# Kernel optimization log

Hardware: AMD Instinct MI355X
Metric: run time of the kernel (lower is better)

The kernel has to match this reference:

```python
import jax, jax.numpy as jnp
import numpy as np

N_BINS = 15
NUM_CLASSES = 16


def _risk_from_H2(u):
    # torch: 0.5*(1 - sqrt(clamp(2*2^-u - 1, min=0)))
    inner = 2.0 * jnp.exp2(-u) - 1.0
    pos = inner > 0.0
    s = jnp.sqrt(jnp.where(pos, inner, 1.0))  # safe sqrt (grad 0 where clamped)
    return 0.5 * (1.0 - jnp.where(pos, s, 0.0))


def setup_inputs() -> dict:
    key = jax.random.key(0)
    k1, k2 = jax.random.split(key)
    N = 4194304
    logits = jax.random.normal(k1, (N, NUM_CLASSES), dtype=jnp.float32)
    labels = jax.random.randint(k2, (N,), 0, NUM_CLASSES)
    return {"logits": logits, "labels": labels}


def reference(logits, labels):
    # logits: [N, C]; labels: [N]
    probs = jax.nn.softmax(logits, axis=-1)                     # [N, C]
    H2 = -jnp.log2((probs * probs).sum(-1) + 1e-12)             # [N]
    err_real = (jnp.argmax(probs, axis=-1) != labels).astype(H2.dtype)  # [N]

    # equal-frequency edges on detached H2 (linear-interp quantiles, as torch.quantile)
    q = jnp.linspace(0.0, 1.0, N_BINS + 1)
    edges = jnp.quantile(jax.lax.stop_gradient(H2), q)
    edges = edges.at[-1].add(1e-6)
    lo, hi = edges[:-1], edges[1:]                              # [n_bins]

    # vectorized replacement of the per-bin Python loop: [n_bins, N] mask
    mask = (H2[None, :] > lo[:, None]) & (H2[None, :] <= hi[:, None])
    maskf = mask.astype(H2.dtype)
    cnt = maskf.sum(-1)                                         # [n_bins]
    safe = jnp.maximum(cnt, 1.0)
    u_bar = (maskf @ H2) / safe                                 # masked means
    err_bar = (maskf @ err_real) / safe
    gaps = jnp.where(cnt > 0.0, jnp.abs(err_bar - _risk_from_H2(u_bar)), 0.0)
    return gaps.mean()
```

## Files before the change

kernel.cpp:

```cpp
#include <hip/hip_runtime.h>

#define L1_BINS 8192
#define L2_BINS 512
#define KEY_MAX 4194303u
#define NH2_BLOCKS 1280
#define NREF_BLOCKS 512
#define NBIN_BLOCKS 256

struct Ranks { unsigned int r[32]; };
struct Fracs { float f[16]; };

__global__ __launch_bounds__(256) void k_zero(uint4* __restrict__ p, int n4) {
  int i = blockIdx.x * blockDim.x + threadIdx.x;
  if (i < n4) p[i] = make_uint4(0u, 0u, 0u, 0u);
}

__global__ __launch_bounds__(256) void k_h2(const float* __restrict__ logits,
                                            const int* __restrict__ labels,
                                            unsigned int* __restrict__ keys,
                                            unsigned int* __restrict__ histg,
                                            int n) {
  __shared__ unsigned int lh[L1_BINS];
  for (int i = threadIdx.x; i < L1_BINS; i += blockDim.x) lh[i] = 0u;
  __syncthreads();
  int tid = blockIdx.x * blockDim.x + threadIdx.x;
  int sub = tid & 3;
  int group = tid >> 2;
  int ngroups = (gridDim.x * blockDim.x) >> 2;
  for (int row = group; row < n; row += ngroups) {
    float4 v = reinterpret_cast<const float4*>(logits)[(size_t)row * 4 + sub];
    float m = v.x; int a = 0;
    if (v.y > m) { m = v.y; a = 1; }
    if (v.z > m) { m = v.z; a = 2; }
    if (v.w > m) { m = v.w; a = 3; }
    int gidx = sub * 4 + a;
#pragma unroll
    for (int mask = 1; mask <= 2; mask <<= 1) {
      float om = __shfl_xor(m, mask);
      int oi = __shfl_xor(gidx, mask);
      if (om > m || (om == m && oi < gidx)) { m = om; gidx = oi; }
    }
    float e0 = __expf(v.x - m), e1 = __expf(v.y - m);
    float e2 = __expf(v.z - m), e3 = __expf(v.w - m);
    float Z = e0 + e1 + e2 + e3;
    float S2 = e0 * e0 + e1 * e1 + e2 * e2 + e3 * e3;
#pragma unroll
    for (int mask = 1; mask <= 2; mask <<= 1) {
      Z += __shfl_xor(Z, mask);
      S2 += __shfl_xor(S2, mask);
    }
    if (sub == 0) {
      float r = S2 / (Z * Z) + 1e-12f;
      float h2 = -__log2f(r);
      int ki = (int)(h2 * 1048576.0f);
      unsigned int key = (unsigned int)min(max(ki, 0), (int)KEY_MAX);
      unsigned int err = (gidx != labels[row]) ? 0x80000000u : 0u;
      keys[row] = key | err;
      atomicAdd(&lh[key >> 9], 1u);
    }
  }
  __syncthreads();
  unsigned int* dst = histg + (size_t)blockIdx.x * (L1_BINS / 2);
  for (int i = threadIdx.x; i < L1_BINS / 2; i += blockDim.x)
    dst[i] = (lh[2 * i] & 0xFFFFu) | (lh[2 * i + 1] << 16);
}

__global__ __launch_bounds__(256) void k_merge(const unsigned int* __restrict__ histg,
                                               unsigned int* __restrict__ merged,
                                               int nrows) {
  __shared__ unsigned int slo[16][17], shi[16][17];
  int col0 = blockIdx.x * 16;
  int c = threadIdx.x & 15;
  int rg = threadIdx.x >> 4;
  unsigned int alo = 0, ahi = 0;
  for (int r = rg; r < nrows; r += 16) {
    unsigned int v = histg[(size_t)r * (L1_BINS / 2) + col0 + c];
    alo += v & 0xFFFFu;
    ahi += v >> 16;
  }
  slo[rg][c] = alo;
  shi[rg][c] = ahi;
  __syncthreads();
  if (threadIdx.x < 16) {
    unsigned int lo = 0, hi = 0;
#pragma unroll
    for (int g = 0; g < 16; ++g) { lo += slo[g][threadIdx.x]; hi += shi[g][threadIdx.x]; }
    int pc = col0 + threadIdx.x;
    merged[2 * pc] = lo;
    merged[2 * pc + 1] = hi;
  }
}

__global__ void k_select(const unsigned int* __restrict__ hist,
                         unsigned int* __restrict__ selpfx,
                         unsigned int* __restrict__ selrank,
                         float* __restrict__ vout,
                         int nb, int perq, int shift, int last, int first,
                         Ranks rk) {
  int j = blockIdx.x;
  int lane = threadIdx.x;
  const unsigned int* h = hist + (perq ? (size_t)j * (size_t)nb : (size_t)0);
  unsigned int rem = first ? rk.r[j] : selrank[j];
  int base = 0, len = nb;
  while (len > 64) {
    int chunk = (len + 63) >> 6;
    int start = base + lane * chunk;
    int end = base + len;
    unsigned int s = 0;
    for (int t = 0; t < chunk; ++t) {
      int idx = start + t;
      if (idx < end) s += h[idx];
    }
    unsigned int inc = s;
#pragma unroll
    for (int d = 1; d < 64; d <<= 1) {
      unsigned int u = __shfl_up(inc, d);
      if (lane >= d) inc += u;
    }
    unsigned int ex = inc - s;
    bool own = (rem >= ex) && (rem < ex + s);
    unsigned long long bal = __ballot(own);
    int src = __ffsll((long long)bal) - 1;
    unsigned int exs = __shfl(ex, src);
    int nbase = base + src * chunk;
    len = min(chunk, end - nbase);
    base = nbase;
    rem -= exs;
  }
  unsigned int s = (lane < len) ? h[base + lane] : 0u;
  unsigned int inc = s;
#pragma unroll
  for (int d = 1; d < 64; d <<= 1) {
    unsigned int u = __shfl_up(inc, d);
    if (lane >= d) inc += u;
  }
  unsigned int ex = inc - s;
  bool own = (rem >= ex) && (rem < ex + s);
  unsigned long long bal = __ballot(own);
  int src = __ffsll((long long)bal) - 1;
  unsigned int exs = __shfl(ex, src);
  if (lane == 0) {
    unsigned int idx = (unsigned int)(base + src);
    unsigned int pfx = first ? idx : ((selpfx[j] << shift) | idx);
    selpfx[j] = pfx;
    selrank[j] = rem - exs;
    if (last) vout[j] = __uint_as_float(pfx);
  }
}

__global__ __launch_bounds__(256) void k_refine(const unsigned int* __restrict__ keys,
                                                const unsigned int* __restrict__ selpfx,
                                                unsigned int* __restrict__ hist2,
                                                int n) {
  __shared__ unsigned int sp[32];
  if (threadIdx.x < 32) sp[threadIdx.x] = selpfx[threadIdx.x];
  __syncthreads();
  int stride = gridDim.x * blockDim.x;
  for (int i = blockIdx.x * blockDim.x + threadIdx.x; i < n; i += stride) {
    unsigned int key = keys[i] & KEY_MAX;
    unsigned int hi = key >> 9;
    unsigned int sub = key & (L2_BINS - 1);
#pragma unroll
    for (int jj = 0; jj < 32; ++jj) {
      if (hi == sp[jj]) atomicAdd(&hist2[jj * L2_BINS + (int)sub], 1u);
    }
  }
}

__global__ __launch_bounds__(256) void k_bin(const unsigned int* __restrict__ keys,
                                             const float* __restrict__ vp,
                                             float* __restrict__ partials,
                                             unsigned int* __restrict__ done,
                                             float* __restrict__ out, int n,
                                             Fracs fr) {
  __shared__ float sedge[16];
  __shared__ float swacc[4][48];
  __shared__ unsigned int is_last;
  if (threadIdx.x < 16) {
    int i = threadIdx.x;
    unsigned int klo = __float_as_uint(vp[2 * i]);
    unsigned int khi = __float_as_uint(vp[2 * i + 1]);
    float lo = (float)(klo + 1u) * 0x1p-20f;
    float hi = (float)(khi + 1u) * 0x1p-20f;
    float f = fr.f[i];
    float e = lo * (1.0f - f) + hi * f;
    if (i == 15) e += 1e-6f;
    sedge[i] = e;
  }
  __syncthreads();
  float e[16];
#pragma unroll
  for (int j = 0; j < 16; ++j) e[j] = sedge[j];
  float cnt[15], sH[15], sE[15];
#pragma unroll
  for (int b = 0; b < 15; ++b) { cnt[b] = 0.f; sH[b] = 0.f; sE[b] = 0.f; }
  int stride = gridDim.x * blockDim.x;
  for (int i = blockIdx.x * blockDim.x + threadIdx.x; i < n; i += stride) {
    unsigned int kp = keys[i];
    float h = ((float)(kp & KEY_MAX) + 0.5f) * 0x1p-20f;
    float er = (kp & 0x80000000u) ? 1.0f : 0.0f;
    int less = 0;
#pragma unroll
    for (int j = 0; j < 16; ++j) less += (h > e[j]) ? 1 : 0;
    int bin = less - 1;
#pragma unroll
    for (int b = 0; b < 15; ++b) {
      bool m = (bin == b);
      cnt[b] += m ? 1.f : 0.f;
      sH[b] += m ? h : 0.f;
      sE[b] += m ? er : 0.f;
    }
  }
  int wid = threadIdx.x >> 6;
  int lane = threadIdx.x & 63;
#pragma unroll
  for (int b = 0; b < 15; ++b) {
    float c = cnt[b], a = sH[b], s = sE[b];
    for (int off = 32; off > 0; off >>= 1) {
      c += __shfl_xor(c, off);
      a += __shfl_xor(a, off);
      s += __shfl_xor(s, off);
    }
    if (lane == 0) {
      swacc[wid][b] = c;
      swacc[wid][15 + b] = a;
      swacc[wid][30 + b] = s;
    }
  }
  __syncthreads();
  if (threadIdx.x < 45) {
    int v = threadIdx.x;
    float s = swacc[0][v] + swacc[1][v] + swacc[2][v] + swacc[3][v];
    partials[v * NBIN_BLOCKS + blockIdx.x] = s;
  }
  __threadfence();
  if (threadIdx.x == 0)
    is_last = (atomicAdd(done, 1u) == (unsigned int)gridDim.x - 1u) ? 1u : 0u;
  __syncthreads();
  if (is_last && threadIdx.x < 64) {
    __shared__ float sacc[45];
    int l = threadIdx.x;
    for (int v = 0; v < 45; ++v) {
      float s = 0.f;
      for (int b = l; b < NBIN_BLOCKS; b += 64) s += partials[v * NBIN_BLOCKS + b];
      for (int off = 32; off > 0; off >>= 1) s += __shfl_xor(s, off);
      if (l == 0) sacc[v] = s;
    }
    __builtin_amdgcn_s_barrier();
    float g = 0.f;
    if (l < 15) {
      float c = sacc[l], sh = sacc[15 + l], se = sacc[30 + l];
      float safe = fmaxf(c, 1.f);
      float u = sh / safe, eb = se / safe;
      float inner = 2.0f * exp2f(-u) - 1.0f;
      float s = (inner > 0.f) ? sqrtf(inner) : 0.f;
      float risk = 0.5f * (1.0f - s);
      g = (c > 0.f) ? fabsf(eb - risk) : 0.f;
    }
    for (int off = 32; off > 0; off >>= 1) g += __shfl_xor(g, off);
    if (l == 0) out[0] = g * (1.0f / 15.0f);
  }
}

extern "C" void kernel_launch(void* const* d_in, const int* in_sizes, int n_in,
                              void* d_out, int out_size, void* d_ws, size_t ws_size,
                              hipStream_t stream) {
  const float* logits = (const float*)d_in[0];
  const int* labels = (const int*)d_in[1];
  float* out = (float*)d_out;
  int n = in_sizes[1];

  char* ws = (char*)d_ws;
  size_t offKeys = 0;
  size_t offHg = (size_t)n * 4;
  size_t offMerged = offHg + (size_t)NH2_BLOCKS * (L1_BINS / 2) * 4;
  size_t offH2b = offMerged + (size_t)L1_BINS * 4;
  size_t offDone = offH2b + 32 * L2_BINS * 4;
  size_t zeroEnd = offDone + 16;
  size_t offSelP = zeroEnd;
  size_t offSelR = offSelP + 128;
  size_t offV = offSelR + 128;
  size_t offPart = (offV + 128 + 255) & ~(size_t)255;

  unsigned int* keys = (unsigned int*)(ws + offKeys);
  unsigned int* histg = (unsigned int*)(ws + offHg);
  unsigned int* merged = (unsigned int*)(ws + offMerged);
  unsigned int* hist2 = (unsigned int*)(ws + offH2b);
  unsigned int* done = (unsigned int*)(ws + offDone);
  unsigned int* selp = (unsigned int*)(ws + offSelP);
  unsigned int* selr = (unsigned int*)(ws + offSelR);
  float* vp = (float*)(ws + offV);
  float* part = (float*)(ws + offPart);

  Ranks rk;
  Fracs fr;
  float nm1 = (float)(n - 1);
  for (int i = 0; i < 16; ++i) {
    float q = (i == 15) ? 1.0f : (float)i * (1.0f / 15.0f);
    float idxf = q * nm1;
    float flo = floorf(idxf);
    unsigned int klo = (unsigned int)flo;
    unsigned int khi = (unsigned int)ceilf(idxf);
    unsigned int maxi = (unsigned int)(n - 1);
    if (klo > maxi) klo = maxi;
    if (khi > maxi) khi = maxi;
    rk.r[2 * i] = klo;
    rk.r[2 * i + 1] = khi;
    fr.f[i] = idxf - flo;
  }

  int zero4 = (int)((zeroEnd - offH2b) >> 4);
  k_zero<<<(zero4 + 255) / 256, 256, 0, stream>>>((uint4*)(ws + offH2b), zero4);
  k_h2<<<NH2_BLOCKS, 256, 0, stream>>>(logits, labels, keys, histg, n);
  k_merge<<<L1_BINS / 2 / 16, 256, 0, stream>>>(histg, merged, NH2_BLOCKS);
  k_select<<<32, 64, 0, stream>>>(merged, selp, selr, vp, L1_BINS, 0, 0, 0, 1, rk);
  k_refine<<<NREF_BLOCKS, 256, 0, stream>>>(keys, selp, hist2, n);
  k_select<<<32, 64, 0, stream>>>(hist2, selp, selr, vp, L2_BINS, 1, 9, 1, 0, rk);
  k_bin<<<NBIN_BLOCKS, 256, 0, stream>>>(keys, vp, part, done, out, n, fr);

  (void)n_in; (void)out_size; (void)ws_size;
}
```

Baseline: 317.1 us.

## Fuse select passes into merge/refine via last-block pattern, rebalance histogram bins

Removes the zero kernel and both standalone select kernels. Zeroing of counters and the level-2 histogram moves into k_h2 and k_merge, and each radix-select step runs in the last-arriving block of k_merge or k_refine, detected with an atomic counter. The L1 histogram shrinks to 4096 bins packed two per uint, written with one atomic per row, and L2 grows to 1024 bins. Grid sizes for the h2, refine and bin kernels go up. This cuts launch count and serialization, at the cost of more per-block histogram partials to merge and tail work done by a single block.

```diff
diff --git a/kernel.cpp b/kernel.cpp
--- a/kernel.cpp
+++ b/kernel.cpp
@@ -1,32 +1,41 @@
 #include <hip/hip_runtime.h>
 
-#define L1_BINS 8192
-#define L2_BINS 512
+#define L1_BINS 4096
+#define L1_UINTS 2048
+#define L2_BINS 1024
 #define KEY_MAX 4194303u
-#define NH2_BLOCKS 1280
-#define NREF_BLOCKS 512
-#define NBIN_BLOCKS 256
+#define NH2_BLOCKS 2048
+#define NMG_BLOCKS 256
+#define NREF_BLOCKS 2048
+#define NBIN_BLOCKS 1024
 
 struct Ranks { unsigned int r[32]; };
 struct Fracs { float f[16]; };
 
-__global__ __launch_bounds__(256) void k_zero(uint4* __restrict__ p, int n4) {
-  int i = blockIdx.x * blockDim.x + threadIdx.x;
-  if (i < n4) p[i] = make_uint4(0u, 0u, 0u, 0u);
+__device__ __forceinline__ unsigned int wave_iscan(unsigned int s, int lane) {
+  unsigned int inc = s;
+#pragma unroll
+  for (int d = 1; d < 64; d <<= 1) {
+    unsigned int u = __shfl_up(inc, d);
+    if (lane >= d) inc += u;
+  }
+  return inc;
 }
 
 __global__ __launch_bounds__(256) void k_h2(const float* __restrict__ logits,
                                             const int* __restrict__ labels,
                                             unsigned int* __restrict__ keys,
                                             unsigned int* __restrict__ histg,
+                                            unsigned int* __restrict__ dones,
                                             int n) {
-  __shared__ unsigned int lh[L1_BINS];
-  for (int i = threadIdx.x; i < L1_BINS; i += blockDim.x) lh[i] = 0u;
-  __syncthreads();
-  int tid = blockIdx.x * blockDim.x + threadIdx.x;
+  __shared__ unsigned int lh[L1_UINTS];
+  for (int i = threadIdx.x; i < L1_UINTS; i += 256) lh[i] = 0u;
+  if (blockIdx.x == 0 && threadIdx.x < 3) dones[threadIdx.x] = 0u;
+  __syncthreads();
+  int tid = blockIdx.x * 256 + threadIdx.x;
   int sub = tid & 3;
   int group = tid >> 2;
-  int ngroups = (gridDim.x * blockDim.x) >> 2;
+  int ngroups = (gridDim.x * 256) >> 2;
   for (int row = group; row < n; row += ngroups) {
     float4 v = reinterpret_cast<const float4*>(logits)[(size_t)row * 4 + sub];
     float m = v.x; int a = 0;
@@ -54,123 +63,132 @@
       float h2 = -__log2f(r);
       int ki = (int)(h2 * 1048576.0f);
       unsigned int key = (unsigned int)min(max(ki, 0), (int)KEY_MAX);
-      unsigned int err = (gidx != labels[row]) ? 0x80000000u : 0u;
-      keys[row] = key | err;
-      atomicAdd(&lh[key >> 9], 1u);
-    }
-  }
-  __syncthreads();
-  unsigned int* dst = histg + (size_t)blockIdx.x * (L1_BINS / 2);
-  for (int i = threadIdx.x; i < L1_BINS / 2; i += blockDim.x)
-    dst[i] = (lh[2 * i] & 0xFFFFu) | (lh[2 * i + 1] << 16);
+      keys[row] = key | ((gidx != labels[row]) ? 0x80000000u : 0u);
+      atomicAdd(&lh[key >> 11], ((key >> 10) & 1u) ? 65536u : 1u);
+    }
+  }
+  __syncthreads();
+  unsigned int* dst = histg + (size_t)blockIdx.x * L1_UINTS;
+  for (int i = threadIdx.x; i < L1_UINTS; i += 256) dst[i] = lh[i];
 }
 
 __global__ __launch_bounds__(256) void k_merge(const unsigned int* __restrict__ histg,
                                                unsigned int* __restrict__ merged,
-                                               int nrows) {
-  __shared__ unsigned int slo[16][17], shi[16][17];
-  int col0 = blockIdx.x * 16;
-  int c = threadIdx.x & 15;
-  int rg = threadIdx.x >> 4;
+                                               unsigned int* __restrict__ hist2,
+                                               unsigned int* __restrict__ dones,
+                                               unsigned int* __restrict__ selpfx,
+                                               unsigned int* __restrict__ selrank,
+                                               Ranks rk) {
+  __shared__ unsigned int slo[32][9], shi[32][9];
+  __shared__ unsigned int is_last;
+  for (int i = threadIdx.x; i < 128; i += 256)
+    hist2[blockIdx.x * 128 + i] = 0u;
+  int col0 = blockIdx.x * 8;
+  int c = threadIdx.x & 7;
+  int rg = threadIdx.x >> 3;
   unsigned int alo = 0, ahi = 0;
-  for (int r = rg; r < nrows; r += 16) {
-    unsigned int v = histg[(size_t)r * (L1_BINS / 2) + col0 + c];
+  for (int r = rg; r < NH2_BLOCKS; r += 32) {
+    unsigned int v = histg[(size_t)r * L1_UINTS + col0 + c];
     alo += v & 0xFFFFu;
     ahi += v >> 16;
   }
   slo[rg][c] = alo;
   shi[rg][c] = ahi;
   __syncthreads();
-  if (threadIdx.x < 16) {
+  if (threadIdx.x < 8) {
     unsigned int lo = 0, hi = 0;
 #pragma unroll
-    for (int g = 0; g < 16; ++g) { lo += slo[g][threadIdx.x]; hi += shi[g][threadIdx.x]; }
+    for (int g = 0; g < 32; ++g) { lo += slo[g][threadIdx.x]; hi += shi[g][threadIdx.x]; }
     int pc = col0 + threadIdx.x;
     merged[2 * pc] = lo;
     merged[2 * pc + 1] = hi;
   }
-}
-
-__global__ void k_select(const unsigned int* __restrict__ hist,
-                         unsigned int* __restrict__ selpfx,
-                         unsigned int* __restrict__ selrank,
-                         float* __restrict__ vout,
-                         int nb, int perq, int shift, int last, int first,
-                         Ranks rk) {
-  int j = blockIdx.x;
-  int lane = threadIdx.x;
-  const unsigned int* h = hist + (perq ? (size_t)j * (size_t)nb : (size_t)0);
-  unsigned int rem = first ? rk.r[j] : selrank[j];
-  int base = 0, len = nb;
-  while (len > 64) {
-    int chunk = (len + 63) >> 6;
-    int start = base + lane * chunk;
-    int end = base + len;
+  __threadfence();
+  __syncthreads();
+  if (threadIdx.x == 0)
+    is_last = (atomicAdd(&dones[0], 1u) == (unsigned int)gridDim.x - 1u) ? 1u : 0u;
+  __syncthreads();
+  if (!is_last) return;
+  __threadfence();
+  int wid = threadIdx.x >> 6, lane = threadIdx.x & 63;
+  for (int j = wid; j < 32; j += 4) {
+    unsigned int rem = rk.r[j];
+    const unsigned int* mp = merged + lane * 64;
     unsigned int s = 0;
-    for (int t = 0; t < chunk; ++t) {
-      int idx = start + t;
-      if (idx < end) s += h[idx];
-    }
-    unsigned int inc = s;
-#pragma unroll
-    for (int d = 1; d < 64; d <<= 1) {
-      unsigned int u = __shfl_up(inc, d);
-      if (lane >= d) inc += u;
-    }
+#pragma unroll 8
+    for (int t = 0; t < 64; ++t) s += mp[t];
+    unsigned int inc = wave_iscan(s, lane);
     unsigned int ex = inc - s;
     bool own = (rem >= ex) && (rem < ex + s);
-    unsigned long long bal = __ballot(own);
-    int src = __ffsll((long long)bal) - 1;
-    unsigned int exs = __shfl(ex, src);
-    int nbase = base + src * chunk;
-    len = min(chunk, end - nbase);
-    base = nbase;
-    rem -= exs;
-  }
-  unsigned int s = (lane < len) ? h[base + lane] : 0u;
-  unsigned int inc = s;
-#pragma unroll
-  for (int d = 1; d < 64; d <<= 1) {
-    unsigned int u = __shfl_up(inc, d);
-    if (lane >= d) inc += u;
-  }
-  unsigned int ex = inc - s;
-  bool own = (rem >= ex) && (rem < ex + s);
-  unsigned long long bal = __ballot(own);
-  int src = __ffsll((long long)bal) - 1;
-  unsigned int exs = __shfl(ex, src);
-  if (lane == 0) {
-    unsigned int idx = (unsigned int)(base + src);
-    unsigned int pfx = first ? idx : ((selpfx[j] << shift) | idx);
-    selpfx[j] = pfx;
-    selrank[j] = rem - exs;
-    if (last) vout[j] = __uint_as_float(pfx);
+    int src = __ffsll((long long)__ballot(own)) - 1;
+    rem -= __shfl(ex, src);
+    int base = src * 64;
+    unsigned int v2 = merged[base + lane];
+    unsigned int inc2 = wave_iscan(v2, lane);
+    unsigned int ex2 = inc2 - v2;
+    bool own2 = (rem >= ex2) && (rem < ex2 + v2);
+    int s2 = __ffsll((long long)__ballot(own2)) - 1;
+    unsigned int ex2s = __shfl(ex2, s2);
+    if (lane == 0) {
+      selpfx[j] = (unsigned int)(base + s2);
+      selrank[j] = rem - ex2s;
+    }
   }
 }
 
 __global__ __launch_bounds__(256) void k_refine(const unsigned int* __restrict__ keys,
                                                 const unsigned int* __restrict__ selpfx,
                                                 unsigned int* __restrict__ hist2,
+                                                unsigned int* __restrict__ dones,
+                                                unsigned int* __restrict__ selrank,
+                                                unsigned int* __restrict__ vout,
                                                 int n) {
   __shared__ unsigned int sp[32];
+  __shared__ unsigned int is_last;
   if (threadIdx.x < 32) sp[threadIdx.x] = selpfx[threadIdx.x];
   __syncthreads();
   int stride = gridDim.x * blockDim.x;
   for (int i = blockIdx.x * blockDim.x + threadIdx.x; i < n; i += stride) {
     unsigned int key = keys[i] & KEY_MAX;
-    unsigned int hi = key >> 9;
-    unsigned int sub = key & (L2_BINS - 1);
-#pragma unroll
-    for (int jj = 0; jj < 32; ++jj) {
-      if (hi == sp[jj]) atomicAdd(&hist2[jj * L2_BINS + (int)sub], 1u);
-    }
+    unsigned int hi = key >> 10;
+    unsigned int sb = key & (L2_BINS - 1);
+#pragma unroll
+    for (int jj = 0; jj < 32; ++jj)
+      if (hi == sp[jj]) atomicAdd(&hist2[jj * L2_BINS + (int)sb], 1u);
+  }
+  __threadfence();
+  __syncthreads();
+  if (threadIdx.x == 0)
+    is_last = (atomicAdd(&dones[1], 1u) == (unsigned int)gridDim.x - 1u) ? 1u : 0u;
+  __syncthreads();
+  if (!is_last) return;
+  __threadfence();
+  int wid = threadIdx.x >> 6, lane = threadIdx.x & 63;
+  for (int j = wid; j < 32; j += 4) {
+    unsigned int rem = selrank[j];
+    const unsigned int* h = hist2 + j * L2_BINS;
+    unsigned int s = 0;
+#pragma unroll
+    for (int t = 0; t < 16; ++t) s += h[lane * 16 + t];
+    unsigned int inc = wave_iscan(s, lane);
+    unsigned int ex = inc - s;
+    bool own = (rem >= ex) && (rem < ex + s);
+    int src = __ffsll((long long)__ballot(own)) - 1;
+    rem -= __shfl(ex, src);
+    unsigned int v2 = (lane < 16) ? h[src * 16 + lane] : 0u;
+    unsigned int inc2 = wave_iscan(v2, lane);
+    unsigned int ex2 = inc2 - v2;
+    bool own2 = (lane < 16) && (rem >= ex2) && (rem < ex2 + v2);
+    int s2 = __ffsll((long long)__ballot(own2)) - 1;
+    if (lane == 0)
+      vout[j] = (sp[j] << 10) | (unsigned int)(src * 16 + s2);
   }
 }
 
 __global__ __launch_bounds__(256) void k_bin(const unsigned int* __restrict__ keys,
-                                             const float* __restrict__ vp,
+                                             const unsigned int* __restrict__ vp,
                                              float* __restrict__ partials,
-                                             unsigned int* __restrict__ done,
+                                             unsigned int* __restrict__ dones,
                                              float* __restrict__ out, int n,
                                              Fracs fr) {
   __shared__ float sedge[16];
@@ -178,8 +196,8 @@
   __shared__ unsigned int is_last;
   if (threadIdx.x < 16) {
     int i = threadIdx.x;
-    unsigned int klo = __float_as_uint(vp[2 * i]);
-    unsigned int khi = __float_as_uint(vp[2 * i + 1]);
+    unsigned int klo = vp[2 * i];
+    unsigned int khi = vp[2 * i + 1];
     float lo = (float)(klo + 1u) * 0x1p-20f;
     float hi = (float)(khi + 1u) * 0x1p-20f;
     float f = fr.f[i];
@@ -205,10 +223,10 @@
     int bin = less - 1;
 #pragma unroll
     for (int b = 0; b < 15; ++b) {
-      bool m = (bin == b);
-      cnt[b] += m ? 1.f : 0.f;
-      sH[b] += m ? h : 0.f;
-      sE[b] += m ? er : 0.f;
+      bool mm = (bin == b);
+      cnt[b] += mm ? 1.f : 0.f;
+      sH[b] += mm ? h : 0.f;
+      sE[b] += mm ? er : 0.f;
     }
   }
   int wid = threadIdx.x >> 6;
@@ -234,10 +252,12 @@
     partials[v * NBIN_BLOCKS + blockIdx.x] = s;
   }
   __threadfence();
+  __syncthreads();
   if (threadIdx.x == 0)
-    is_last = (atomicAdd(done, 1u) == (unsigned int)gridDim.x - 1u) ? 1u : 0u;
+    is_last = (atomicAdd(&dones[2], 1u) == (unsigned int)gridDim.x - 1u) ? 1u : 0u;
   __syncthreads();
   if (is_last && threadIdx.x < 64) {
+    __threadfence();
     __shared__ float sacc[45];
     int l = threadIdx.x;
     for (int v = 0; v < 45; ++v) {
@@ -273,11 +293,10 @@
   char* ws = (char*)d_ws;
   size_t offKeys = 0;
   size_t offHg = (size_t)n * 4;
-  size_t offMerged = offHg + (size_t)NH2_BLOCKS * (L1_BINS / 2) * 4;
+  size_t offMerged = offHg + (size_t)NH2_BLOCKS * L1_UINTS * 4;
   size_t offH2b = offMerged + (size_t)L1_BINS * 4;
-  size_t offDone = offH2b + 32 * L2_BINS * 4;
-  size_t zeroEnd = offDone + 16;
-  size_t offSelP = zeroEnd;
+  size_t offDone = offH2b + (size_t)32 * L2_BINS * 4;
+  size_t offSelP = offDone + 16;
   size_t offSelR = offSelP + 128;
   size_t offV = offSelR + 128;
   size_t offPart = (offV + 128 + 255) & ~(size_t)255;
@@ -286,10 +305,10 @@
   unsigned int* histg = (unsigned int*)(ws + offHg);
   unsigned int* merged = (unsigned int*)(ws + offMerged);
   unsigned int* hist2 = (unsigned int*)(ws + offH2b);
-  unsigned int* done = (unsigned int*)(ws + offDone);
+  unsigned int* dones = (unsigned int*)(ws + offDone);
   unsigned int* selp = (unsigned int*)(ws + offSelP);
   unsigned int* selr = (unsigned int*)(ws + offSelR);
-  float* vp = (float*)(ws + offV);
+  unsigned int* vp = (unsigned int*)(ws + offV);
   float* part = (float*)(ws + offPart);
 
   Ranks rk;
@@ -309,14 +328,10 @@
     fr.f[i] = idxf - flo;
   }
 
-  int zero4 = (int)((zeroEnd - offH2b) >> 4);
-  k_zero<<<(zero4 + 255) / 256, 256, 0, stream>>>((uint4*)(ws + offH2b), zero4);
-  k_h2<<<NH2_BLOCKS, 256, 0, stream>>>(logits, labels, keys, histg, n);
-  k_merge<<<L1_BINS / 2 / 16, 256, 0, stream>>>(histg, merged, NH2_BLOCKS);
-  k_select<<<32, 64, 0, stream>>>(merged, selp, selr, vp, L1_BINS, 0, 0, 0, 1, rk);
-  k_refine<<<NREF_BLOCKS, 256, 0, stream>>>(keys, selp, hist2, n);
-  k_select<<<32, 64, 0, stream>>>(hist2, selp, selr, vp, L2_BINS, 1, 9, 1, 0, rk);
-  k_bin<<<NBIN_BLOCKS, 256, 0, stream>>>(keys, vp, part, done, out, n, fr);
+  k_h2<<<NH2_BLOCKS, 256, 0, stream>>>(logits, labels, keys, histg, dones, n);
+  k_merge<<<NMG_BLOCKS, 256, 0, stream>>>(histg, merged, hist2, dones, selp, selr, rk);
+  k_refine<<<NREF_BLOCKS, 256, 0, stream>>>(keys, selp, hist2, dones, selr, vp, n);
+  k_bin<<<NBIN_BLOCKS, 256, 0, stream>>>(keys, vp, part, dones, out, n, fr);
 
   (void)n_in; (void)out_size; (void)ws_size;
 }
```

After: 540.5 us. 1.7x slower.
